# Kernel tuning notes

Hardware: AMD Instinct MI355X
Metric: run time of the kernel (lower is better)

## Reference

```python
import jax, jax.numpy as jnp
import numpy as np

IN_F, OUT_F, BATCH = 4096, 11008, 8

def setup_inputs() -> dict:
    key = jax.random.key(0)
    k_x, k_s, k_sg, k_b = jax.random.split(key, 4)
    x = jax.random.normal(k_x, (BATCH, IN_F), dtype=jnp.float32)
    # stored codes in [1, 255] as in QINSCodec.encode (uint8 storage)
    stored = jax.random.randint(k_s, (OUT_F, IN_F), 1, 256, dtype=jnp.int32).astype(jnp.uint8)
    # sign in {-1, +1} (int8 storage)
    sign = (jax.random.randint(k_sg, (OUT_F, IN_F), 0, 2, dtype=jnp.int32) * 2 - 1).astype(jnp.int8)
    log_min = jnp.array([-10.0], dtype=jnp.float32)
    log_max = jnp.array([0.0], dtype=jnp.float32)
    bias = jax.random.normal(k_b, (OUT_F,), dtype=jnp.float32) * 0.02
    return {"x": x, "stored": stored, "sign": sign, "log_min": log_min, "log_max": log_max, "bias": bias}

def _decode(stored, sign, log_min, log_max):
    # QINSCodec.decode: normalized = (255 - stored)/254; w = sign * exp(log_min + normalized*(log_max-log_min))
    normalized = (255.0 - stored.astype(jnp.float32)) / 254.0
    log_w = log_min + normalized * (log_max - log_min)
    return sign.astype(jnp.float32) * jnp.exp(log_w)

def reference(x, stored, sign, log_min, log_max, bias):
    lmin = log_min[0]
    lmax = log_max[0]
    w = _decode(stored, sign, lmin, lmax)            # [OUT_F, IN_F]
    return x @ w.T + bias                            # F.linear(x, w, bias)
```

## Files before the change

kernel.cpp:

```cpp
#include <hip/hip_runtime.h>
#include <stdint.h>

#define IN_F   4096
#define OUT_F  11008
#define BATCH  8
#define WAVES  4
#define RPW    2
#define RPB    (WAVES*RPW)
#define CHUNK  128
#define NCHUNK (IN_F/CHUNK)
#define SLOTI  (3*RPB*CHUNK)

typedef __attribute__((address_space(1))) const uint32_t* gas_t;
typedef __attribute__((address_space(3))) uint32_t* las_t;

#define DMA16(gsrc, ldst) \
    __builtin_amdgcn_global_load_lds((gas_t)(gsrc), (las_t)(ldst), 16, 0, 0)

__device__ __forceinline__ float qins_decode(int code, int sgn, float d0, float d1) {
    const float e = __builtin_amdgcn_exp2f(fmaf((float)code, d1, d0));
    const uint32_t m = ((uint32_t)sgn) & 0x80000000u;
    return __uint_as_float(__float_as_uint(e) ^ m);
}

__global__ __launch_bounds__(256, 4)
void qins_linear_kernel(const float* __restrict__ x,
                        const uint32_t* __restrict__ stored,
                        const uint32_t* __restrict__ sign,
                        const float* __restrict__ log_min,
                        const float* __restrict__ log_max,
                        const float* __restrict__ bias,
                        float* __restrict__ out)
{
    __shared__ int lds[2][SLOTI];

    const int tid  = threadIdx.x;
    const int lane = tid & 63;
    const int wave = tid >> 6;
    const int o0   = blockIdx.x * RPB;

    const float lmin = log_min[0];
    const float lmax = log_max[0];
    const float L2E  = 1.44269504088896340736f;
    const float d1 = -(lmax - lmin) * (L2E / 254.0f);
    const float d0 = (lmin + (lmax - lmin) * (255.0f / 254.0f)) * L2E;

    const int sub = lane >> 5;
    const int i32 = (lane & 31) * 4;
    const uint32_t* gs = stored + (size_t)(o0 + 2 * wave + sub) * IN_F + i32;
    const uint32_t* gg = sign   + (size_t)(o0 + 2 * wave + sub) * IN_F + i32;
    const uint32_t* gx = (const uint32_t*)x + (size_t)(2 * wave + sub) * IN_F + i32;

    float acc[RPW][BATCH];
#pragma unroll
    for (int r = 0; r < RPW; ++r)
#pragma unroll
        for (int b = 0; b < BATCH; ++b) acc[r][b] = 0.0f;

    {
        DMA16(gs, &lds[0][wave * 256]);
        DMA16(gg, &lds[0][1024 + wave * 256]);
        DMA16(gx, &lds[0][2048 + wave * 256]);
    }
    __syncthreads();

#pragma unroll 1
    for (int k = 0; k < NCHUNK; ++k) {
        const int cur = k & 1;
        if (k + 1 < NCHUNK) {
            const int nxt = cur ^ 1;
            const int ip  = (k + 1) * CHUNK;
            DMA16(gs + ip, &lds[nxt][wave * 256]);
            DMA16(gg + ip, &lds[nxt][1024 + wave * 256]);
            DMA16(gx + ip, &lds[nxt][2048 + wave * 256]);
        }

        {
            const int li = lane * 2;
            const int2 c0 = *reinterpret_cast<const int2*>(&lds[cur][wave * 256 + li]);
            const int2 c1 = *reinterpret_cast<const int2*>(&lds[cur][wave * 256 + 128 + li]);
            const int2 g0 = *reinterpret_cast<const int2*>(&lds[cur][1024 + wave * 256 + li]);
            const int2 g1 = *reinterpret_cast<const int2*>(&lds[cur][1024 + wave * 256 + 128 + li]);
            const float w00 = qins_decode(c0.x, g0.x, d0, d1);
            const float w01 = qins_decode(c0.y, g0.y, d0, d1);
            const float w10 = qins_decode(c1.x, g1.x, d0, d1);
            const float w11 = qins_decode(c1.y, g1.y, d0, d1);
#pragma unroll
            for (int b = 0; b < BATCH; ++b) {
                const float2 xv = *reinterpret_cast<const float2*>(
                    &lds[cur][2048 + (b >> 1) * 256 + (b & 1) * 128 + li]);
                acc[0][b] = fmaf(w01, xv.y, fmaf(w00, xv.x, acc[0][b]));
                acc[1][b] = fmaf(w11, xv.y, fmaf(w10, xv.x, acc[1][b]));
            }
        }
        __syncthreads();
    }

#pragma unroll
    for (int r = 0; r < RPW; ++r)
#pragma unroll
        for (int b = 0; b < BATCH; ++b) {
            float v = acc[r][b];
#pragma unroll
            for (int s = 32; s >= 1; s >>= 1)
                v += __shfl_xor(v, s, 64);
            acc[r][b] = v;
        }

    if (lane == 0) {
#pragma unroll
        for (int r = 0; r < RPW; ++r) {
            const int row = o0 + 2 * wave + r;
            const float bv = bias[row];
#pragma unroll
            for (int b = 0; b < BATCH; ++b)
                out[(size_t)b * OUT_F + row] = acc[r][b] + bv;
        }
    }
}

extern "C" void kernel_launch(void* const* d_in, const int* in_sizes, int n_in,
                              void* d_out, int out_size, void* d_ws, size_t ws_size,
                              hipStream_t stream)
{
    const float*    x      = (const float*)d_in[0];
    const uint32_t* stored = (const uint32_t*)d_in[1];
    const uint32_t* sign   = (const uint32_t*)d_in[2];
    const float*    lmin   = (const float*)d_in[3];
    const float*    lmax   = (const float*)d_in[4];
    const float*    bias   = (const float*)d_in[5];
    float* out = (float*)d_out;

    dim3 grid(OUT_F / RPB), block(WAVES * 64);
    qins_linear_kernel<<<grid, block, 0, stream>>>(x, stored, sign, lmin, lmax, bias, out);
}
```

Before: 72.83 us.

## Deepen LDS DMA pipeline to four slots with explicit vmcnt waits

Replaces the double-buffered global-to-LDS DMA loop with a four-slot ring that keeps three chunks in flight. Each iteration uses explicit s_waitcnt vmcnt counts and a single barrier instead of a full syncthreads after compute, so memory latency overlaps more compute. LDS use doubles and the launch-bounds occupancy hint drops from 4 to 3 blocks, which trades occupancy for deeper prefetch in a memory-bound GEMV.

```diff
diff --git a/kernel.cpp b/kernel.cpp
--- a/kernel.cpp
+++ b/kernel.cpp
@@ -9,6 +9,7 @@
 #define RPB    (WAVES*RPW)
 #define CHUNK  128
 #define NCHUNK (IN_F/CHUNK)
+#define NSLOT  4
 #define SLOTI  (3*RPB*CHUNK)
 
 typedef __attribute__((address_space(1))) const uint32_t* gas_t;
@@ -17,13 +18,20 @@
 #define DMA16(gsrc, ldst) \
     __builtin_amdgcn_global_load_lds((gas_t)(gsrc), (las_t)(ldst), 16, 0, 0)
 
+#define SBAR() __builtin_amdgcn_sched_barrier(0)
+#define VWAIT(N)                                                             \
+    do {                                                                     \
+        asm volatile("s_waitcnt vmcnt(" #N ")" ::: "memory");                \
+        SBAR();                                                              \
+    } while (0)
+
 __device__ __forceinline__ float qins_decode(int code, int sgn, float d0, float d1) {
     const float e = __builtin_amdgcn_exp2f(fmaf((float)code, d1, d0));
     const uint32_t m = ((uint32_t)sgn) & 0x80000000u;
     return __uint_as_float(__float_as_uint(e) ^ m);
 }
 
-__global__ __launch_bounds__(256, 4)
+__global__ __launch_bounds__(256, 3)
 void qins_linear_kernel(const float* __restrict__ x,
                         const uint32_t* __restrict__ stored,
                         const uint32_t* __restrict__ sign,
@@ -32,7 +40,7 @@
                         const float* __restrict__ bias,
                         float* __restrict__ out)
 {
-    __shared__ int lds[2][SLOTI];
+    __shared__ int lds[NSLOT][SLOTI];
 
     const int tid  = threadIdx.x;
     const int lane = tid & 63;
@@ -51,32 +59,40 @@
     const uint32_t* gg = sign   + (size_t)(o0 + 2 * wave + sub) * IN_F + i32;
     const uint32_t* gx = (const uint32_t*)x + (size_t)(2 * wave + sub) * IN_F + i32;
 
+#define ISSUE(T, K)                                                          \
+    do {                                                                     \
+        const int _ip = (K) * CHUNK;                                         \
+        DMA16(gs + _ip, &lds[T][wave * 256]);                                \
+        DMA16(gg + _ip, &lds[T][1024 + wave * 256]);                         \
+        DMA16(gx + _ip, &lds[T][2048 + wave * 256]);                         \
+    } while (0)
+
     float acc[RPW][BATCH];
 #pragma unroll
     for (int r = 0; r < RPW; ++r)
 #pragma unroll
         for (int b = 0; b < BATCH; ++b) acc[r][b] = 0.0f;
 
-    {
-        DMA16(gs, &lds[0][wave * 256]);
-        DMA16(gg, &lds[0][1024 + wave * 256]);
-        DMA16(gx, &lds[0][2048 + wave * 256]);
-    }
-    __syncthreads();
+    ISSUE(0, 0);
+    ISSUE(1, 1);
+    ISSUE(2, 2);
+    SBAR();
 
 #pragma unroll 1
     for (int k = 0; k < NCHUNK; ++k) {
-        const int cur = k & 1;
-        if (k + 1 < NCHUNK) {
-            const int nxt = cur ^ 1;
-            const int ip  = (k + 1) * CHUNK;
-            DMA16(gs + ip, &lds[nxt][wave * 256]);
-            DMA16(gg + ip, &lds[nxt][1024 + wave * 256]);
-            DMA16(gx + ip, &lds[nxt][2048 + wave * 256]);
-        }
+        if (k < NCHUNK - 2)       VWAIT(6);
+        else if (k == NCHUNK - 2) VWAIT(3);
+        else                      VWAIT(0);
+        __builtin_amdgcn_s_barrier();
+        SBAR();
+
+        if (k + 3 < NCHUNK)
+            ISSUE((k + 3) & (NSLOT - 1), k + 3);
+        SBAR();
 
         {
-            const int li = lane * 2;
+            const int cur = k & (NSLOT - 1);
+            const int li  = lane * 2;
             const int2 c0 = *reinterpret_cast<const int2*>(&lds[cur][wave * 256 + li]);
             const int2 c1 = *reinterpret_cast<const int2*>(&lds[cur][wave * 256 + 128 + li]);
             const int2 g0 = *reinterpret_cast<const int2*>(&lds[cur][1024 + wave * 256 + li]);
@@ -93,7 +109,6 @@
                 acc[1][b] = fmaf(w11, xv.y, fmaf(w10, xv.x, acc[1][b]));
             }
         }
-        __syncthreads();
     }
 
 #pragma unroll
@@ -117,6 +132,7 @@
                 out[(size_t)b * OUT_F + row] = acc[r][b] + bv;
         }
     }
+#undef ISSUE
 }
 
 extern "C" void kernel_launch(void* const* d_in, const int* in_sizes, int n_in,
```

After: 78.64 us. +8.0%, slower.

## Split-K over four slices with eight rows per wave and atomic accumulation

Applied to the files above, without the earlier changes.

Each wave now handles eight output rows, so every x value loaded from LDS is reused across eight rows instead of two. The input dimension is split into four slices across blocks, which gives a larger grid. Partial sums are combined with float atomicAdd into an output that a separate init kernel first fills with the bias. This adds a second kernel launch and atomic traffic, makes the summation order nondeterministic, and raises register pressure from 64 accumulators per thread.

```diff
diff --git a/kernel.cpp b/kernel.cpp
--- a/kernel.cpp
+++ b/kernel.cpp
@@ -5,11 +5,13 @@
 #define OUT_F  11008
 #define BATCH  8
 #define WAVES  4
-#define RPW    2
+#define RPW    8
 #define RPB    (WAVES*RPW)
-#define CHUNK  128
-#define NCHUNK (IN_F/CHUNK)
-#define SLOTI  (3*RPB*CHUNK)
+#define NS     4
+#define SLICE  (IN_F/NS)
+#define CHUNK  64
+#define NCHUNK (SLICE/CHUNK)
+#define SLOTI  (2*RPB*CHUNK + BATCH*CHUNK)
 
 typedef __attribute__((address_space(1))) const uint32_t* gas_t;
 typedef __attribute__((address_space(3))) uint32_t* las_t;
@@ -23,21 +25,32 @@
     return __uint_as_float(__float_as_uint(e) ^ m);
 }
 
+__global__ void qins_init(const float* __restrict__ bias, float* __restrict__ out)
+{
+    const int o = blockIdx.x * 256 + threadIdx.x;
+    const float bv = bias[o];
+#pragma unroll
+    for (int b = 0; b < BATCH; ++b)
+        out[(size_t)b * OUT_F + o] = bv;
+}
+
 __global__ __launch_bounds__(256, 4)
-void qins_linear_kernel(const float* __restrict__ x,
-                        const uint32_t* __restrict__ stored,
-                        const uint32_t* __restrict__ sign,
-                        const float* __restrict__ log_min,
-                        const float* __restrict__ log_max,
-                        const float* __restrict__ bias,
-                        float* __restrict__ out)
+void qins_main(const float* __restrict__ x,
+               const uint32_t* __restrict__ stored,
+               const uint32_t* __restrict__ sign,
+               const float* __restrict__ log_min,
+               const float* __restrict__ log_max,
+               float* __restrict__ out)
 {
     __shared__ int lds[2][SLOTI];
 
     const int tid  = threadIdx.x;
     const int lane = tid & 63;
     const int wave = tid >> 6;
-    const int o0   = blockIdx.x * RPB;
+    const int rg   = blockIdx.x % (OUT_F / RPB);
+    const int s    = blockIdx.x / (OUT_F / RPB);
+    const int o0   = rg * RPB;
+    const int i0   = s * SLICE;
 
     const float lmin = log_min[0];
     const float lmax = log_max[0];
@@ -45,11 +58,25 @@
     const float d1 = -(lmax - lmin) * (L2E / 254.0f);
     const float d0 = (lmin + (lmax - lmin) * (255.0f / 254.0f)) * L2E;
 
-    const int sub = lane >> 5;
-    const int i32 = (lane & 31) * 4;
-    const uint32_t* gs = stored + (size_t)(o0 + 2 * wave + sub) * IN_F + i32;
-    const uint32_t* gg = sign   + (size_t)(o0 + 2 * wave + sub) * IN_F + i32;
-    const uint32_t* gx = (const uint32_t*)x + (size_t)(2 * wave + sub) * IN_F + i32;
+    const int rsub = lane >> 4;
+    const int csub = (lane & 15) * 4;
+    const uint32_t* gsA = stored + (size_t)(o0 + 8 * wave + rsub) * IN_F + i0 + csub;
+    const uint32_t* gsB = gsA + 4 * IN_F;
+    const uint32_t* ggA = sign   + (size_t)(o0 + 8 * wave + rsub) * IN_F + i0 + csub;
+    const uint32_t* ggB = ggA + 4 * IN_F;
+    const uint32_t* gxw = (const uint32_t*)x
+                        + (size_t)((wave & 1) * 4 + rsub) * IN_F + i0 + csub;
+
+#define ISSUE(T, K)                                                          \
+    do {                                                                     \
+        const int _ip = (K) * CHUNK;                                         \
+        DMA16(gsA + _ip, &lds[T][wave * 512]);                               \
+        DMA16(gsB + _ip, &lds[T][wave * 512 + 256]);                         \
+        DMA16(ggA + _ip, &lds[T][2048 + wave * 512]);                        \
+        DMA16(ggB + _ip, &lds[T][2048 + wave * 512 + 256]);                  \
+        if (wave < 2)                                                        \
+            DMA16(gxw + _ip, &lds[T][4096 + wave * 256]);                    \
+    } while (0)
 
     float acc[RPW][BATCH];
 #pragma unroll
@@ -57,40 +84,29 @@
 #pragma unroll
         for (int b = 0; b < BATCH; ++b) acc[r][b] = 0.0f;
 
-    {
-        DMA16(gs, &lds[0][wave * 256]);
-        DMA16(gg, &lds[0][1024 + wave * 256]);
-        DMA16(gx, &lds[0][2048 + wave * 256]);
-    }
+    ISSUE(0, 0);
     __syncthreads();
 
 #pragma unroll 1
     for (int k = 0; k < NCHUNK; ++k) {
         const int cur = k & 1;
-        if (k + 1 < NCHUNK) {
-            const int nxt = cur ^ 1;
-            const int ip  = (k + 1) * CHUNK;
-            DMA16(gs + ip, &lds[nxt][wave * 256]);
-            DMA16(gg + ip, &lds[nxt][1024 + wave * 256]);
-            DMA16(gx + ip, &lds[nxt][2048 + wave * 256]);
-        }
+        if (k + 1 < NCHUNK)
+            ISSUE(cur ^ 1, k + 1);
 
         {
-            const int li = lane * 2;
-            const int2 c0 = *reinterpret_cast<const int2*>(&lds[cur][wave * 256 + li]);
-            const int2 c1 = *reinterpret_cast<const int2*>(&lds[cur][wave * 256 + 128 + li]);
-            const int2 g0 = *reinterpret_cast<const int2*>(&lds[cur][1024 + wave * 256 + li]);
-            const int2 g1 = *reinterpret_cast<const int2*>(&lds[cur][1024 + wave * 256 + 128 + li]);
-            const float w00 = qins_decode(c0.x, g0.x, d0, d1);
-            const float w01 = qins_decode(c0.y, g0.y, d0, d1);
-            const float w10 = qins_decode(c1.x, g1.x, d0, d1);
-            const float w11 = qins_decode(c1.y, g1.y, d0, d1);
+            float w8[RPW];
+#pragma unroll
+            for (int r = 0; r < RPW; ++r) {
+                const int c_ = lds[cur][wave * 512 + r * 64 + lane];
+                const int g_ = lds[cur][2048 + wave * 512 + r * 64 + lane];
+                w8[r] = qins_decode(c_, g_, d0, d1);
+            }
 #pragma unroll
             for (int b = 0; b < BATCH; ++b) {
-                const float2 xv = *reinterpret_cast<const float2*>(
-                    &lds[cur][2048 + (b >> 1) * 256 + (b & 1) * 128 + li]);
-                acc[0][b] = fmaf(w01, xv.y, fmaf(w00, xv.x, acc[0][b]));
-                acc[1][b] = fmaf(w11, xv.y, fmaf(w10, xv.x, acc[1][b]));
+                const float xv = __int_as_float(lds[cur][4096 + b * 64 + lane]);
+#pragma unroll
+                for (int r = 0; r < RPW; ++r)
+                    acc[r][b] = fmaf(w8[r], xv, acc[r][b]);
             }
         }
         __syncthreads();
@@ -102,21 +118,21 @@
         for (int b = 0; b < BATCH; ++b) {
             float v = acc[r][b];
 #pragma unroll
-            for (int s = 32; s >= 1; s >>= 1)
-                v += __shfl_xor(v, s, 64);
+            for (int sft = 32; sft >= 1; sft >>= 1)
+                v += __shfl_xor(v, sft, 64);
             acc[r][b] = v;
         }
 
     if (lane == 0) {
 #pragma unroll
         for (int r = 0; r < RPW; ++r) {
-            const int row = o0 + 2 * wave + r;
-            const float bv = bias[row];
+            const int row = o0 + 8 * wave + r;
 #pragma unroll
             for (int b = 0; b < BATCH; ++b)
-                out[(size_t)b * OUT_F + row] = acc[r][b] + bv;
+                atomicAdd(out + (size_t)b * OUT_F + row, acc[r][b]);
         }
     }
+#undef ISSUE
 }
 
 extern "C" void kernel_launch(void* const* d_in, const int* in_sizes, int n_in,
@@ -131,6 +147,7 @@
     const float*    bias   = (const float*)d_in[5];
     float* out = (float*)d_out;
 
-    dim3 grid(OUT_F / RPB), block(WAVES * 64);
-    qins_linear_kernel<<<grid, block, 0, stream>>>(x, stored, sign, lmin, lmax, bias, out);
+    qins_init<<<dim3(OUT_F / 256), dim3(256), 0, stream>>>(bias, out);
+    qins_main<<<dim3((OUT_F / RPB) * NS), dim3(256), 0, stream>>>(
+        x, stored, sign, lmin, lmax, out);
 }
```

After: 96.75 us. 1.33x slower.
